# Optimization experiments

Measured on AMD Instinct MI355X. Metric: run time of the kernel, lower is better.

Reference implementation:

```python
import jax, jax.numpy as jnp
import numpy as np

B, W, H, L, D = 4, 32, 32, 32, 256
K, S, V = 24, 16384, 8  # heads, selected positions per head, logits per head
N = B * W * H * L


def setup_inputs() -> dict:
    key = jax.random.key(0)
    k1, k2, k3, k4, k5 = jax.random.split(key, 5)
    block_type_grid = jax.random.randint(k1, (B, W, H, L), 0, 800, dtype=jnp.int32)
    features = jax.random.normal(k2, (B, W, H, L, D), dtype=jnp.float32)
    mask_idx = jax.random.randint(k3, (K, S), 0, N, dtype=jnp.int32)
    head_weights = jax.random.normal(k4, (K, D, V), dtype=jnp.float32) * (1.0 / np.sqrt(D))
    head_bias = jax.random.normal(k5, (K, V), dtype=jnp.float32) * 0.01
    return {
        "block_type_grid": block_type_grid,
        "features": features,
        "mask_idx": mask_idx,
        "head_weights": head_weights,
        "head_bias": head_bias,
    }


def reference(block_type_grid, features, mask_idx, head_weights, head_bias):
    # Flatten spatial grid: (B,W,H,L,D) -> (N,D)
    feats_flat = features.reshape(-1, D)
    # Grouped boolean-mask gather (as fixed-size index gather): (K,S,D)
    gathered = feats_flat[mask_idx]
    # Per-head small Linear: logits[k,s,v] = gathered[k,s,:] @ W[k,:,v] + b[k,v]
    logits = jnp.einsum('ksd,kdv->ksv', gathered, head_weights) + head_bias[:, None, :]
    return logits
```

## Files before the change

kernel.cpp:

```cpp
#include <hip/hip_runtime.h>


#define KH 24
#define SS 16384
#define VV 8
#define DD 256
#define NROW 131072
#define NE (KH * SS)

typedef __attribute__((ext_vector_type(8))) short s16x8;
typedef __attribute__((ext_vector_type(4))) float f32x4;
typedef __attribute__((ext_vector_type(4))) unsigned int u32x4;

__device__ __forceinline__ unsigned short rne_bf16(float f) {
    unsigned u = __builtin_bit_cast(unsigned, f);
    unsigned r = u + 0x7FFFu + ((u >> 16) & 1u);
    return (unsigned short)(r >> 16);
}
__device__ __forceinline__ float bf16f(unsigned short h) {
    unsigned u = ((unsigned)h) << 16;
    return __builtin_bit_cast(float, u);
}

template <int CTRL>
__device__ __forceinline__ float dpp_mov(float x) {
    int xi = __builtin_bit_cast(int, x);
    int r = __builtin_amdgcn_update_dpp(xi, xi, CTRL, 0xF, 0xF, false);
    return __builtin_bit_cast(float, r);
}

__global__ __launch_bounds__(256) void wk_kernel(
    const float* __restrict__ head_w, unsigned short* __restrict__ whi,
    unsigned short* __restrict__ wlo)
{
    const int idx = blockIdx.x * 256 + threadIdx.x;
    const int j = idx & 7, lane = (idx >> 3) & 63;
    const int kb = (idx >> 9) & 7, hp = idx >> 12;
    const int head = hp * 2 + ((lane & 15) >> 3);
    const int v = lane & 7;
    const int k = kb * 32 + (lane >> 4) * 8 + j;
    const float f = head_w[((size_t)head * DD + k) * VV + v];
    const unsigned short hi = rne_bf16(f);
    whi[idx] = hi;
    wlo[idx] = rne_bf16(f - bf16f(hi));
}

__global__ __launch_bounds__(256, 4) void mkd_kernel(
    const float* __restrict__ feats,
    const unsigned short* __restrict__ whi,
    const unsigned short* __restrict__ wlo,
    float* __restrict__ logits)
{
    const int tid  = threadIdx.x;
    const int wave = tid >> 6;
    const int lane = tid & 63;
    const int m    = lane & 15;
    const int kq   = lane >> 4;
    const int r0   = blockIdx.x * 64;

    __shared__ unsigned short Bbuf[2][8192];

    const float* arow = feats + ((size_t)(r0 + wave * 16 + m)) * DD + kq * 8;
    s16x8 ahi[8], alo[8];
#pragma unroll
    for (int kb = 0; kb < 8; ++kb) {
        const float4 p = *(const float4*)(arow + kb * 32);
        const float4 q = *(const float4*)(arow + kb * 32 + 4);
        const float fv[8] = {p.x, p.y, p.z, p.w, q.x, q.y, q.z, q.w};
        s16x8 h, l;
#pragma unroll
        for (int j = 0; j < 8; ++j) {
            const unsigned short hi = rne_bf16(fv[j]);
            h[j] = (short)hi;
            l[j] = (short)rne_bf16(fv[j] - bf16f(hi));
        }
        u32x4 ph = __builtin_bit_cast(u32x4, h);
        u32x4 pl = __builtin_bit_cast(u32x4, l);
        asm volatile("" : "+v"(ph), "+v"(pl));
        ahi[kb] = __builtin_bit_cast(s16x8, ph);
        alo[kb] = __builtin_bit_cast(s16x8, pl);
    }

    {
        const uint4* sh = (const uint4*)(whi);
        const uint4* sl = (const uint4*)(wlo);
        uint4* bb = (uint4*)(&Bbuf[0][0]);
        bb[tid]       = sh[tid];
        bb[256 + tid] = sh[256 + tid];
        bb[512 + tid] = sl[tid];
        bb[768 + tid] = sl[256 + tid];
    }
    __syncthreads();

    for (int hp = 0; hp < 12; ++hp) {
        const int cur = hp & 1;

        uint4 t0, t1, t2, t3;
        const bool pf = (hp + 1) < 12;
        if (pf) {
            const uint4* sh = (const uint4*)(whi + (hp + 1) * 4096);
            const uint4* sl = (const uint4*)(wlo + (hp + 1) * 4096);
            t0 = sh[tid]; t1 = sh[256 + tid];
            t2 = sl[tid]; t3 = sl[256 + tid];
        }

        f32x4 c0 = {0.f, 0.f, 0.f, 0.f};
        f32x4 c1 = {0.f, 0.f, 0.f, 0.f};
#pragma unroll
        for (int kb = 0; kb < 8; kb += 2) {
            const s16x8 bh0 = *(const s16x8*)(&Bbuf[cur][kb * 512 + lane * 8]);
            const s16x8 bl0 = *(const s16x8*)(&Bbuf[cur][4096 + kb * 512 + lane * 8]);
            const s16x8 bh1 = *(const s16x8*)(&Bbuf[cur][(kb + 1) * 512 + lane * 8]);
            const s16x8 bl1 = *(const s16x8*)(&Bbuf[cur][4096 + (kb + 1) * 512 + lane * 8]);
            c0 = __builtin_amdgcn_mfma_f32_16x16x32_bf16(ahi[kb], bh0, c0, 0, 0, 0);
            c1 = __builtin_amdgcn_mfma_f32_16x16x32_bf16(ahi[kb + 1], bh1, c1, 0, 0, 0);
            c0 = __builtin_amdgcn_mfma_f32_16x16x32_bf16(alo[kb], bh0, c0, 0, 0, 0);
            c1 = __builtin_amdgcn_mfma_f32_16x16x32_bf16(alo[kb + 1], bh1, c1, 0, 0, 0);
            c0 = __builtin_amdgcn_mfma_f32_16x16x32_bf16(ahi[kb], bl0, c0, 0, 0, 0);
            c1 = __builtin_amdgcn_mfma_f32_16x16x32_bf16(ahi[kb + 1], bl1, c1, 0, 0, 0);
        }
        const f32x4 c = c0 + c1;

        float* Lp = logits + ((size_t)hp * NROW + (r0 + wave * 16 + kq * 4)) * 16 + m;
#pragma unroll
        for (int rg = 0; rg < 4; ++rg)
            Lp[(size_t)rg * 16] = c[rg];

        if (pf) {
            uint4* bb = (uint4*)(&Bbuf[cur ^ 1][0]);
            bb[tid]       = t0;
            bb[256 + tid] = t1;
            bb[512 + tid] = t2;
            bb[768 + tid] = t3;
            __syncthreads();
        }
    }
}

__global__ __launch_bounds__(256) void gk_kernel(
    const float* __restrict__ logits,
    const int* __restrict__ mask_idx,
    const float* __restrict__ head_b,
    float* __restrict__ out)
{
    const int t = blockIdx.x * 256 + threadIdx.x;
    const int e = t >> 3;
    const int v = t & 7;
    const int k = e >> 14;
    const unsigned row = (unsigned)mask_idx[e];
    const int hp = k >> 1, half = k & 1;
    out[t] = logits[((size_t)hp * NROW + row) * 16 + half * 8 + v]
           + head_b[k * VV + v];
}

__global__ __launch_bounds__(256) void attr_decoder_fallback(
    const float* __restrict__ feats, const int* __restrict__ mask_idx,
    const float* __restrict__ head_w, const float* __restrict__ head_b,
    float* __restrict__ out)
{
    const int lane  = threadIdx.x & 63;
    const int wv    = __builtin_amdgcn_readfirstlane(threadIdx.x >> 6);
    const int k     = blockIdx.x >> 7;
    const int chunk = blockIdx.x & 127;
    const int lb    = lane & 7;

    const float* Wk = head_w + (size_t)k * (DD * VV);
    float w[4][8];
    {
        const bool q0 = (lane & 1) != 0;
        const bool q1 = (lane & 2) != 0;
        const bool q2 = (lane & 4) != 0;
#pragma unroll
        for (int t = 0; t < 4; ++t) {
            const float4 a = *(const float4*)(Wk + (lane * 4 + t) * VV);
            const float4 b = *(const float4*)(Wk + (lane * 4 + t) * VV + 4);
            const float x[8] = {a.x, a.y, a.z, a.w, b.x, b.y, b.z, b.w};
            float y[8], z[8];
#pragma unroll
            for (int j = 0; j < 8; ++j) y[j] = q0 ? x[j ^ 1] : x[j];
#pragma unroll
            for (int j = 0; j < 8; ++j) z[j] = q1 ? y[j ^ 2] : y[j];
#pragma unroll
            for (int j = 0; j < 8; ++j) w[t][j] = q2 ? z[j ^ 4] : z[j];
        }
    }
    const float bias = head_b[k * VV + lb];

    const char* fb = (const char*)feats;
    const int s_base = chunk * 128 + wv * 32;
    const int* mi = mask_idx + k * SS + s_base;
    float* outp = out + ((size_t)k * SS + s_base) * VV;
    const int vo = lane << 4;

    int4 rows = *(const int4*)mi;
    int r0 = __builtin_amdgcn_readfirstlane(rows.x);
    int r1 = __builtin_amdgcn_readfirstlane(rows.y);
    int r2 = __builtin_amdgcn_readfirstlane(rows.z);
    int r3 = __builtin_amdgcn_readfirstlane(rows.w);

    for (int i = 0; i < 32; i += 4) {
        const float4 f0 = *(const float4*)(fb + (((size_t)(unsigned)r0) << 10) + vo);
        const float4 f1 = *(const float4*)(fb + (((size_t)(unsigned)r1) << 10) + vo);
        const float4 f2 = *(const float4*)(fb + (((size_t)(unsigned)r2) << 10) + vo);
        const float4 f3 = *(const float4*)(fb + (((size_t)(unsigned)r3) << 10) + vo);
        if (i < 28) rows = *(const int4*)(mi + i + 4);

        float r[4];
        const float4 f[4] = {f0, f1, f2, f3};
#pragma unroll
        for (int u = 0; u < 4; ++u) {
            float acc[8];
#pragma unroll
            for (int v = 0; v < 8; ++v) {
                acc[v] = f[u].x * w[0][v];
                acc[v] = fmaf(f[u].y, w[1][v], acc[v]);
                acc[v] = fmaf(f[u].z, w[2][v], acc[v]);
                acc[v] = fmaf(f[u].w, w[3][v], acc[v]);
            }
            const float a40 = acc[0] + dpp_mov<0xB1>(acc[1]);
            const float a41 = acc[2] + dpp_mov<0xB1>(acc[3]);
            const float a42 = acc[4] + dpp_mov<0xB1>(acc[5]);
            const float a43 = acc[6] + dpp_mov<0xB1>(acc[7]);
            const float a20 = a40 + dpp_mov<0x4E>(a41);
            const float a21 = a42 + dpp_mov<0x4E>(a43);
            r[u] = a20 + __shfl_xor(a21, 4, 64);
        }
        r0 = __builtin_amdgcn_readfirstlane(rows.x);
        r1 = __builtin_amdgcn_readfirstlane(rows.y);
        r2 = __builtin_amdgcn_readfirstlane(rows.z);
        r3 = __builtin_amdgcn_readfirstlane(rows.w);

        const bool b3 = (lane & 8) != 0;
        const bool b4 = (lane & 16) != 0;
        const float t0 = (b3 ? r[1] : r[0]) + dpp_mov<0x128>(b3 ? r[0] : r[1]);
        const float t1 = (b3 ? r[3] : r[2]) + dpp_mov<0x128>(b3 ? r[2] : r[3]);
        float va = (b4 ? t1 : t0) + __shfl_xor(b4 ? t0 : t1, 16, 64);
        va += __shfl_xor(va, 32, 64);
        if (lane < 32) outp[i * VV + lane] = va + bias;
    }
}

extern "C" void kernel_launch(void* const* d_in, const int* in_sizes, int n_in,
                              void* d_out, int out_size, void* d_ws, size_t ws_size,
                              hipStream_t stream) {
    const float* feats    = (const float*)d_in[1];
    const int*   mask_idx = (const int*)  d_in[2];
    const float* head_w   = (const float*)d_in[3];
    const float* head_b   = (const float*)d_in[4];
    float* out = (float*)d_out;

    const size_t need = 100663296u + 2u * 98304u;
    if (d_ws != nullptr && ws_size >= need) {
        char* ws = (char*)d_ws;
        float* logits = (float*)ws;
        unsigned short* whi = (unsigned short*)(ws + 100663296u);
        unsigned short* wlo = (unsigned short*)(ws + 100761600u);

        wk_kernel<<<dim3(192),   dim3(256), 0, stream>>>(head_w, whi, wlo);
        mkd_kernel<<<dim3(2048), dim3(256), 0, stream>>>(feats, whi, wlo, logits);
        gk_kernel<<<dim3(NE * VV / 256), dim3(256), 0, stream>>>(
            logits, mask_idx, head_b, out);
    } else {
        attr_decoder_fallback<<<dim3(KH * 128), dim3(256), 0, stream>>>(
            feats, mask_idx, head_w, head_b, out);
    }
}
```

Measured before the change: 257.5 us.

## Swap GEMM operand roles: keep weights in registers, stage features in swizzled LDS

The dense logits kernel now stages a 32-row feature tile as split bf16 hi/lo in XOR-swizzled shared memory. Each wave holds one head-pair's weight fragments in registers, and each block covers 4 head pairs, so the grid is 3x the row blocks. This removes the serial 12-iteration loop over head pairs with its per-iteration weight double-buffering and barriers, and raises parallelism. In exchange, each feature row is now loaded and converted three times, once per head-pair group, and the tiles are smaller.

```diff
diff --git a/kernel.cpp b/kernel.cpp
--- a/kernel.cpp
+++ b/kernel.cpp
@@ -45,7 +45,7 @@
     wlo[idx] = rne_bf16(f - bf16f(hi));
 }
 
-__global__ __launch_bounds__(256, 4) void mkd_kernel(
+__global__ __launch_bounds__(256, 4) void mks_kernel(
     const float* __restrict__ feats,
     const unsigned short* __restrict__ whi,
     const unsigned short* __restrict__ wlo,
@@ -54,86 +54,81 @@
     const int tid  = threadIdx.x;
     const int wave = tid >> 6;
     const int lane = tid & 63;
-    const int m    = lane & 15;
-    const int kq   = lane >> 4;
-    const int r0   = blockIdx.x * 64;
-
-    __shared__ unsigned short Bbuf[2][8192];
-
-    const float* arow = feats + ((size_t)(r0 + wave * 16 + m)) * DD + kq * 8;
-    s16x8 ahi[8], alo[8];
+    const int bid  = blockIdx.x;
+    const int rb   = bid / 3;
+    const int hpg  = bid - rb * 3;
+    const int hp   = hpg * 4 + wave;
+    const int r0   = rb * 32;
+
+    __shared__ unsigned short Ahi[32 * 256];
+    __shared__ unsigned short Alo[32 * 256];
+
+    {
+        const int row = tid >> 3;
+        const int c8  = tid & 7;
+        const float* src = feats + (size_t)(r0 + row) * DD + c8 * 8;
+        const unsigned sw = ((unsigned)(row & 7)) << 4;
+#pragma unroll
+        for (int i = 0; i < 4; ++i) {
+            const float4 p = *(const float4*)(src + i * 64);
+            const float4 q = *(const float4*)(src + i * 64 + 4);
+            const float fv[8] = {p.x, p.y, p.z, p.w, q.x, q.y, q.z, q.w};
+            s16x8 h, l;
+#pragma unroll
+            for (int j = 0; j < 8; ++j) {
+                const unsigned short hi = rne_bf16(fv[j]);
+                h[j] = (short)hi;
+                l[j] = (short)rne_bf16(fv[j] - bf16f(hi));
+            }
+            const unsigned byteoff = ((unsigned)(row * 512 + c8 * 16 + i * 128)) ^ sw;
+            *(s16x8*)((char*)Ahi + byteoff) = h;
+            *(s16x8*)((char*)Alo + byteoff) = l;
+        }
+    }
+
+    s16x8 Bh[8], Bl[8];
 #pragma unroll
     for (int kb = 0; kb < 8; ++kb) {
-        const float4 p = *(const float4*)(arow + kb * 32);
-        const float4 q = *(const float4*)(arow + kb * 32 + 4);
-        const float fv[8] = {p.x, p.y, p.z, p.w, q.x, q.y, q.z, q.w};
-        s16x8 h, l;
-#pragma unroll
-        for (int j = 0; j < 8; ++j) {
-            const unsigned short hi = rne_bf16(fv[j]);
-            h[j] = (short)hi;
-            l[j] = (short)rne_bf16(fv[j] - bf16f(hi));
-        }
-        u32x4 ph = __builtin_bit_cast(u32x4, h);
-        u32x4 pl = __builtin_bit_cast(u32x4, l);
+        Bh[kb] = *(const s16x8*)(whi + (((size_t)hp * 8 + kb) * 64 + lane) * 8);
+        Bl[kb] = *(const s16x8*)(wlo + (((size_t)hp * 8 + kb) * 64 + lane) * 8);
+        u32x4 ph = __builtin_bit_cast(u32x4, Bh[kb]);
+        u32x4 pl = __builtin_bit_cast(u32x4, Bl[kb]);
         asm volatile("" : "+v"(ph), "+v"(pl));
-        ahi[kb] = __builtin_bit_cast(s16x8, ph);
-        alo[kb] = __builtin_bit_cast(s16x8, pl);
-    }
-
-    {
-        const uint4* sh = (const uint4*)(whi);
-        const uint4* sl = (const uint4*)(wlo);
-        uint4* bb = (uint4*)(&Bbuf[0][0]);
-        bb[tid]       = sh[tid];
-        bb[256 + tid] = sh[256 + tid];
-        bb[512 + tid] = sl[tid];
-        bb[768 + tid] = sl[256 + tid];
-    }
+        Bh[kb] = __builtin_bit_cast(s16x8, ph);
+        Bl[kb] = __builtin_bit_cast(s16x8, pl);
+    }
+
     __syncthreads();
 
-    for (int hp = 0; hp < 12; ++hp) {
-        const int cur = hp & 1;
-
-        uint4 t0, t1, t2, t3;
-        const bool pf = (hp + 1) < 12;
-        if (pf) {
-            const uint4* sh = (const uint4*)(whi + (hp + 1) * 4096);
-            const uint4* sl = (const uint4*)(wlo + (hp + 1) * 4096);
-            t0 = sh[tid]; t1 = sh[256 + tid];
-            t2 = sl[tid]; t3 = sl[256 + tid];
-        }
+    const int m  = lane & 15;
+    const int kq = lane >> 4;
+
+#pragma unroll
+    for (int mt = 0; mt < 2; ++mt) {
+        const int arow = mt * 16 + m;
+        const unsigned abase = ((unsigned)(arow * 512 + kq * 16)) ^ (((unsigned)(arow & 7)) << 4);
 
         f32x4 c0 = {0.f, 0.f, 0.f, 0.f};
         f32x4 c1 = {0.f, 0.f, 0.f, 0.f};
 #pragma unroll
         for (int kb = 0; kb < 8; kb += 2) {
-            const s16x8 bh0 = *(const s16x8*)(&Bbuf[cur][kb * 512 + lane * 8]);
-            const s16x8 bl0 = *(const s16x8*)(&Bbuf[cur][4096 + kb * 512 + lane * 8]);
-            const s16x8 bh1 = *(const s16x8*)(&Bbuf[cur][(kb + 1) * 512 + lane * 8]);
-            const s16x8 bl1 = *(const s16x8*)(&Bbuf[cur][4096 + (kb + 1) * 512 + lane * 8]);
-            c0 = __builtin_amdgcn_mfma_f32_16x16x32_bf16(ahi[kb], bh0, c0, 0, 0, 0);
-            c1 = __builtin_amdgcn_mfma_f32_16x16x32_bf16(ahi[kb + 1], bh1, c1, 0, 0, 0);
-            c0 = __builtin_amdgcn_mfma_f32_16x16x32_bf16(alo[kb], bh0, c0, 0, 0, 0);
-            c1 = __builtin_amdgcn_mfma_f32_16x16x32_bf16(alo[kb + 1], bh1, c1, 0, 0, 0);
-            c0 = __builtin_amdgcn_mfma_f32_16x16x32_bf16(ahi[kb], bl0, c0, 0, 0, 0);
-            c1 = __builtin_amdgcn_mfma_f32_16x16x32_bf16(ahi[kb + 1], bl1, c1, 0, 0, 0);
+            const s16x8 ah0 = *(const s16x8*)((const char*)Ahi + (abase ^ (unsigned)(kb * 64)));
+            const s16x8 al0 = *(const s16x8*)((const char*)Alo + (abase ^ (unsigned)(kb * 64)));
+            const s16x8 ah1 = *(const s16x8*)((const char*)Ahi + (abase ^ (unsigned)((kb + 1) * 64)));
+            const s16x8 al1 = *(const s16x8*)((const char*)Alo + (abase ^ (unsigned)((kb + 1) * 64)));
+            c0 = __builtin_amdgcn_mfma_f32_16x16x32_bf16(ah0, Bh[kb], c0, 0, 0, 0);
+            c1 = __builtin_amdgcn_mfma_f32_16x16x32_bf16(ah1, Bh[kb + 1], c1, 0, 0, 0);
+            c0 = __builtin_amdgcn_mfma_f32_16x16x32_bf16(al0, Bh[kb], c0, 0, 0, 0);
+            c1 = __builtin_amdgcn_mfma_f32_16x16x32_bf16(al1, Bh[kb + 1], c1, 0, 0, 0);
+            c0 = __builtin_amdgcn_mfma_f32_16x16x32_bf16(ah0, Bl[kb], c0, 0, 0, 0);
+            c1 = __builtin_amdgcn_mfma_f32_16x16x32_bf16(ah1, Bl[kb + 1], c1, 0, 0, 0);
         }
         const f32x4 c = c0 + c1;
 
-        float* Lp = logits + ((size_t)hp * NROW + (r0 + wave * 16 + kq * 4)) * 16 + m;
+        float* Lp = logits + ((size_t)hp * NROW + (r0 + mt * 16 + kq * 4)) * 16 + m;
 #pragma unroll
         for (int rg = 0; rg < 4; ++rg)
             Lp[(size_t)rg * 16] = c[rg];
-
-        if (pf) {
-            uint4* bb = (uint4*)(&Bbuf[cur ^ 1][0]);
-            bb[tid]       = t0;
-            bb[256 + tid] = t1;
-            bb[512 + tid] = t2;
-            bb[768 + tid] = t3;
-            __syncthreads();
-        }
     }
 }
 
@@ -256,8 +251,8 @@
         unsigned short* whi = (unsigned short*)(ws + 100663296u);
         unsigned short* wlo = (unsigned short*)(ws + 100761600u);
 
-        wk_kernel<<<dim3(192),   dim3(256), 0, stream>>>(head_w, whi, wlo);
-        mkd_kernel<<<dim3(2048), dim3(256), 0, stream>>>(feats, whi, wlo, logits);
+        wk_kernel<<<dim3(192),        dim3(256), 0, stream>>>(head_w, whi, wlo);
+        mks_kernel<<<dim3(4096 * 3),  dim3(256), 0, stream>>>(feats, whi, wlo, logits);
         gk_kernel<<<dim3(NE * VV / 256), dim3(256), 0, stream>>>(
             logits, mask_idx, head_b, out);
     } else {
```

Result: slower. 283.9 us (+10.2%).
